# Kernel optimization log

Measured on AMD Instinct MI355X. Metric: run time of the kernel, lower is better.

Reference implementation:

```python
import jax, jax.numpy as jnp
import numpy as np

N, E, F_IN, HID, EMB = 100000, 3200000, 128, 16, 8
NEG_SLOPE = 0.2


def _seg_softmax(logits, seg, n):
    # Numerically stable softmax over segments (per trailing channel if 2D).
    m = jax.ops.segment_max(logits, seg, num_segments=n)
    e = jnp.exp(logits - m[seg])
    s = jax.ops.segment_sum(e, seg, num_segments=n)
    return e / s[seg]


def _gatv2(x, src, dst, Wl, Wr, att, bias, t, n):
    # GATv2Conv, heads=1, add_self_loops=False, eval mode (dropout off),
    # with learnable SoftmaxAggregation replacing the sum aggregation.
    xl = x @ Wl                      # [N, C] source transform
    xr = x @ Wr                      # [N, C] target transform
    score = jnp.sum(jax.nn.leaky_relu(xl[src] + xr[dst], NEG_SLOPE) * att, axis=-1)  # [E]
    alpha = _seg_softmax(score, dst, n)          # attention softmax over incoming edges
    m = xl[src] * alpha[:, None]                 # [E, C] messages
    w = _seg_softmax(m * t, dst, n)              # SoftmaxAggregation(learn=True), per channel
    return jax.ops.segment_sum(w * m, dst, num_segments=n) + bias


def setup_inputs() -> dict:
    key = jax.random.key(0)
    ks = iter(jax.random.split(key, 32))
    r = lambda shape, s=0.1: jax.random.normal(next(ks), shape, dtype=jnp.float32) * s
    return dict(
        x=r((N, F_IN), 1.0),
        edge_index=jax.random.randint(next(ks), (2, E), 0, N, dtype=jnp.int32),
        batch=jnp.arange(N, dtype=jnp.int32),
        Wl1=r((F_IN, HID)), Wr1=r((F_IN, HID)), att1=r((HID,)), b1=r((HID,)),
        Wlin1=r((F_IN, HID)), blin1=r((HID,)),
        Wl2=r((HID, EMB)), Wr2=r((HID, EMB)), att2=r((EMB,)), b2=r((EMB,)),
        Wlin2=r((HID, EMB)), blin2=r((EMB,)),
        t=jnp.ones((1,), jnp.float32),
        W3=r((EMB, EMB)), b3=r((EMB,)),
        W4=r((EMB, 1)), b4=r((1,)),
        W5=r((1, 1)), b5=r((1,)),
        Wout=r((1, 1)), bout=r((1,)),
    )


def reference(x, edge_index, batch, Wl1, Wr1, att1, b1, Wlin1, blin1,
              Wl2, Wr2, att2, b2, Wlin2, blin2, t,
              W3, b3, W4, b4, W5, b5, Wout, bout):
    n = x.shape[0]
    src, dst = edge_index[0], edge_index[1]
    # layer 1: GATv2 + skip Linear, relu, global_add_pool
    h = _gatv2(x, src, dst, Wl1, Wr1, att1, b1, t, n) + (x @ Wlin1 + blin1)
    h = jax.nn.relu(h)
    g = jax.ops.segment_sum(h, batch, num_segments=n)  # global_add_pool (batch=arange(N))
    # layer 2: GATv2 + skip Linear on pooled tensor (as in original code), relu, pool
    h2 = _gatv2(g, src, dst, Wl2, Wr2, att2, b2, t, n) + (g @ Wlin2 + blin2)
    h2 = jax.nn.relu(h2)
    g2 = jax.ops.segment_sum(h2, batch, num_segments=n)
    # small MLP head
    z = jax.nn.relu(g2 @ W3 + b3)
    z = jax.nn.relu(z @ W4 + b4)
    z = jax.nn.relu(z @ W5 + b5)
    return jax.nn.log_sigmoid(z @ Wout + bout)
```

## Files before the change

### kernel.cpp

```cpp
#include <hip/hip_runtime.h>
#include <hip/hip_bf16.h>
#include <math.h>

#define F_IN 128
#define C1 16
#define C2 8

#define LBITS 8
#define LOCAL (1 << LBITS)
#define NB_MAX 512
#define ITEMS 16
#define EPB (256 * ITEMS)

static __device__ __forceinline__ unsigned short f2bf(float f) {
  __hip_bfloat16 h = __float2bfloat16(f);
  return *(unsigned short*)&h;
}

__global__ void bucket_hist(const int* __restrict__ dst, int* __restrict__ bcount, int E, int NB) {
  __shared__ int h[NB_MAX];
  for (int i = threadIdx.x; i < NB; i += blockDim.x) h[i] = 0;
  __syncthreads();
  int stride = gridDim.x * blockDim.x;
  for (int e = blockIdx.x * blockDim.x + threadIdx.x; e < E; e += stride)
    atomicAdd(&h[dst[e] >> LBITS], 1);
  __syncthreads();
  for (int i = threadIdx.x; i < NB; i += blockDim.x)
    if (h[i]) atomicAdd(&bcount[i], h[i]);
}

__global__ void bucket_scan(const int* __restrict__ bcount, int* __restrict__ bbase,
                            int* __restrict__ bcursor, int NB) {
  __shared__ int sd[NB_MAX];
  int t = threadIdx.x;
  int v = (t < NB) ? bcount[t] : 0;
  sd[t] = v;
  __syncthreads();
  int acc = v;
  for (int off = 1; off < NB_MAX; off <<= 1) {
    int u = (t >= off) ? sd[t - off] : 0;
    __syncthreads();
    acc += u;
    sd[t] = acc;
    __syncthreads();
  }
  if (t < NB) {
    int excl = acc - v;
    bbase[t] = excl;
    bcursor[t] = excl;
    if (t == NB - 1) bbase[NB] = acc;
  }
}

__global__ __launch_bounds__(256) void phaseA_lds(const int* __restrict__ src,
                                                  const int* __restrict__ dst,
                                                  int* __restrict__ bcursor,
                                                  int* __restrict__ packed, int E, int NB) {
  __shared__ int hist[NB_MAX];
  __shared__ int lbase[NB_MAX];
  __shared__ int gbase[NB_MAX];
  __shared__ int sdata[256];
  __shared__ int stage[EPB];
  __shared__ unsigned short stageb[EPB];
  int t = threadIdx.x;
  for (int i = t; i < NB; i += 256) hist[i] = 0;
  __syncthreads();
  int base = blockIdx.x * EPB;
  int vals[ITEMS];
  int bkt[ITEMS];
#pragma unroll
  for (int k = 0; k < ITEMS; k++) {
    int e = base + k * 256 + t;
    if (e < E) {
      int s = src[e];
      int d = dst[e];
      bkt[k] = d >> LBITS;
      vals[k] = (s << LBITS) | (d & (LOCAL - 1));
      atomicAdd(&hist[bkt[k]], 1);
    } else {
      bkt[k] = -1;
    }
  }
  __syncthreads();
  int i0 = 2 * t, i1 = 2 * t + 1;
  int h0 = (i0 < NB) ? hist[i0] : 0;
  int h1 = (i1 < NB) ? hist[i1] : 0;
  int s2 = h0 + h1;
  sdata[t] = s2;
  __syncthreads();
  int acc = s2;
  for (int off = 1; off < 256; off <<= 1) {
    int u = (t >= off) ? sdata[t - off] : 0;
    __syncthreads();
    acc += u;
    sdata[t] = acc;
    __syncthreads();
  }
  int excl = acc - s2;
  if (i0 < NB) lbase[i0] = excl;
  if (i1 < NB) lbase[i1] = excl + h0;
  __syncthreads();
  for (int i = t; i < NB; i += 256) {
    int c = hist[i];
    gbase[i] = c ? atomicAdd(&bcursor[i], c) : 0;
    hist[i] = lbase[i];
  }
  __syncthreads();
#pragma unroll
  for (int k = 0; k < ITEMS; k++) {
    if (bkt[k] >= 0) {
      int lp = atomicAdd(&hist[bkt[k]], 1);
      stage[lp] = vals[k];
      stageb[lp] = (unsigned short)bkt[k];
    }
  }
  __syncthreads();
  int blockE = E - base;
  if (blockE > EPB) blockE = EPB;
  for (int i = t; i < blockE; i += 256) {
    int b = stageb[i];
    packed[gbase[b] + (i - lbase[b])] = stage[i];
  }
}

__global__ void phaseB_sort(const int* __restrict__ packed, const int* __restrict__ bbase,
                            int* __restrict__ row_ptr, int* __restrict__ ssrc, int N, int E) {
  __shared__ int h[LOCAL];
  __shared__ int sd[LOCAL];
  int b = blockIdx.x;
  int t = threadIdx.x;
  int beg = bbase[b], end = bbase[b + 1];
  int node0 = b << LBITS;
  h[t] = 0;
  __syncthreads();
  for (int j = beg + t; j < end; j += blockDim.x) atomicAdd(&h[packed[j] & (LOCAL - 1)], 1);
  __syncthreads();
  int cnt = h[t];
  sd[t] = cnt;
  __syncthreads();
  int acc = cnt;
  for (int off = 1; off < LOCAL; off <<= 1) {
    int u = (t >= off) ? sd[t - off] : 0;
    __syncthreads();
    acc += u;
    sd[t] = acc;
    __syncthreads();
  }
  int myex = acc - cnt;
  int node = node0 + t;
  if (node < N) row_ptr[node] = beg + myex;
  h[t] = beg + myex;
  if (b == gridDim.x - 1 && t == 0) row_ptr[N] = E;
  __syncthreads();
  for (int j = beg + t; j < end; j += blockDim.x) {
    int v = packed[j];
    int p = atomicAdd(&h[v & (LOCAL - 1)], 1);
    ssrc[p] = v >> LBITS;
  }
}

__global__ __launch_bounds__(256) void gemm3_128x16(
    const float* __restrict__ x, const float* __restrict__ Wl, const float* __restrict__ Wr,
    const float* __restrict__ Wlin, const float* __restrict__ blin,
    __hip_bfloat16* __restrict__ XLh, float* __restrict__ XR, float* __restrict__ SK, int N) {
  int bx = blockIdx.x;
  int mat = bx % 3;
  int node = (bx / 3) * 256 + threadIdx.x;
  if (node >= N) return;
  const float* __restrict__ W = (mat == 0) ? Wl : (mat == 1) ? Wr : Wlin;
  const float4* xr4 = (const float4*)(x + (size_t)node * F_IN);
  float acc[16];
#pragma unroll
  for (int c = 0; c < 16; c++) acc[c] = 0.f;
#pragma unroll 8
  for (int kk = 0; kk < F_IN / 4; kk++) {
    float4 xv = xr4[kk];
    float xs[4] = {xv.x, xv.y, xv.z, xv.w};
#pragma unroll
    for (int j = 0; j < 4; j++) {
      int k = kk * 4 + j;
#pragma unroll
      for (int c = 0; c < 16; c++) acc[c] = fmaf(xs[j], W[k * 16 + c], acc[c]);
    }
  }
  if (mat == 0) {
    unsigned int pk[8];
#pragma unroll
    for (int i = 0; i < 8; i++)
      pk[i] = (unsigned)f2bf(acc[2 * i]) | ((unsigned)f2bf(acc[2 * i + 1]) << 16);
    uint4* xlp = (uint4*)(XLh + (size_t)node * 16);
    xlp[0] = make_uint4(pk[0], pk[1], pk[2], pk[3]);
    xlp[1] = make_uint4(pk[4], pk[5], pk[6], pk[7]);
  } else if (mat == 1) {
    float4* xrp = (float4*)(XR + (size_t)node * 16);
#pragma unroll
    for (int q = 0; q < 4; q++)
      xrp[q] = make_float4(acc[4 * q], acc[4 * q + 1], acc[4 * q + 2], acc[4 * q + 3]);
  } else {
    float4* skp = (float4*)(SK + (size_t)node * 16);
#pragma unroll
    for (int q = 0; q < 4; q++)
      skp[q] = make_float4(acc[4 * q] + blin[4 * q], acc[4 * q + 1] + blin[4 * q + 1],
                           acc[4 * q + 2] + blin[4 * q + 2], acc[4 * q + 3] + blin[4 * q + 3]);
  }
}

template <int C, int POOL, bool HEAD, bool FUSEG2>
__global__ __launch_bounds__(256) void gat_layer(
    const __hip_bfloat16* __restrict__ XLh, const float* __restrict__ XR,
    const float* __restrict__ SK, const float* __restrict__ att, const float* __restrict__ bias,
    const float* __restrict__ tp, const int* __restrict__ row_ptr, const int* __restrict__ ssrc,
    float* __restrict__ H, int N,
    const float* __restrict__ P0, const float* __restrict__ P1, const float* __restrict__ P2,
    const float* __restrict__ P3, const float* __restrict__ P4, const float* __restrict__ P5,
    const float* __restrict__ P6, const float* __restrict__ P7,
    __hip_bfloat16* __restrict__ XL2h, float* __restrict__ XR2, float* __restrict__ SK2,
    float* __restrict__ out) {
  constexpr int NPB = 256 / C;
  constexpr int LOGNPB = (NPB == 16) ? 4 : 5;
  __shared__ __align__(16) unsigned short vpool[POOL * C];
  __shared__ float ppool[POOL];
  __shared__ __align__(16) float xrl[NPB * C];
  __shared__ float invS0s[NPB];
  __shared__ int nb[NPB + 1];
  __shared__ float hsh[(HEAD || FUSEG2) ? NPB * C : 1];
  __shared__ float wfuse[FUSEG2 ? 392 : 1];
  int t = threadIdx.x;
  int node0 = blockIdx.x * NPB;

  if (t <= NPB) {
    int nd = node0 + t;
    nb[t] = row_ptr[(nd < N) ? nd : N];
  }
  {
    size_t xi = (size_t)node0 * C + t;
    xrl[t] = (xi < (size_t)N * C) ? XR[xi] : 0.f;
  }
  if constexpr (FUSEG2) {
    for (int i = t; i < 392; i += 256)
      wfuse[i] = (i < 128) ? P0[i] : (i < 256) ? P1[i - 128] : (i < 384) ? P2[i - 256] : P3[i - 384];
  }
  float attr[C];
#pragma unroll
  for (int cc = 0; cc < C; cc++) attr[cc] = att[cc];
  float tval = tp[0];
  __syncthreads();

  int bbeg = nb[0];
  int nE = nb[NPB] - bbeg;
  int nCap = (nE < POOL) ? nE : POOL;
  const unsigned short* XLu = (const unsigned short*)XLh;

  for (int slot = t; slot < nCap; slot += 256) {
    int sb = slot + bbeg;
    int lo = 0, hi = NPB;
#pragma unroll
    for (int st = 0; st < LOGNPB; st++) {
      int mid = (lo + hi) >> 1;
      bool go = nb[mid] <= sb;
      lo = go ? mid : lo;
      hi = go ? hi : mid;
    }
    int g = lo;
    int s = ssrc[sb];
    float v[C];
    if constexpr (C == 16) {
      const uint4* gp = (const uint4*)(XLu + (size_t)s * 16);
      uint4 a = gp[0], b = gp[1];
      *(uint4*)&vpool[slot * 16] = a;
      *(uint4*)&vpool[slot * 16 + 8] = b;
      unsigned arr[8] = {a.x, a.y, a.z, a.w, b.x, b.y, b.z, b.w};
#pragma unroll
      for (int i = 0; i < 8; i++) {
        v[2 * i] = __uint_as_float(arr[i] << 16);
        v[2 * i + 1] = __uint_as_float(arr[i] & 0xffff0000u);
      }
    } else {
      const uint4* gp = (const uint4*)(XLu + (size_t)s * 8);
      uint4 a = gp[0];
      *(uint4*)&vpool[slot * 8] = a;
      unsigned arr[4] = {a.x, a.y, a.z, a.w};
#pragma unroll
      for (int i = 0; i < 4; i++) {
        v[2 * i] = __uint_as_float(arr[i] << 16);
        v[2 * i + 1] = __uint_as_float(arr[i] & 0xffff0000u);
      }
    }
    float xr[C];
    const float4* xp = (const float4*)&xrl[g * C];
#pragma unroll
    for (int q = 0; q < C / 4; q++) {
      float4 f = xp[q];
      xr[4 * q] = f.x;
      xr[4 * q + 1] = f.y;
      xr[4 * q + 2] = f.z;
      xr[4 * q + 3] = f.w;
    }
    float p0 = 0.f, p1 = 0.f, p2 = 0.f, p3 = 0.f;
#pragma unroll
    for (int cc = 0; cc < C; cc += 4) {
      float u0 = v[cc] + xr[cc];
      float u1 = v[cc + 1] + xr[cc + 1];
      float u2 = v[cc + 2] + xr[cc + 2];
      float u3 = v[cc + 3] + xr[cc + 3];
      p0 = fmaf(fmaxf(u0, 0.2f * u0), attr[cc], p0);
      p1 = fmaf(fmaxf(u1, 0.2f * u1), attr[cc + 1], p1);
      p2 = fmaf(fmaxf(u2, 0.2f * u2), attr[cc + 2], p2);
      p3 = fmaf(fmaxf(u3, 0.2f * u3), attr[cc + 3], p3);
    }
    ppool[slot] = __expf((p0 + p1) + (p2 + p3));
  }
  __syncthreads();

  int g = t / C;
  int c = t % C;
  int base = nb[g] - bbeg;
  int deg = nb[g + 1] - nb[g];
  int capd = POOL - base;
  capd = capd < 0 ? 0 : (capd > deg ? deg : capd);

  {
    float s0 = 0.f;
    for (int j = c; j < capd; j += C) s0 += ppool[base + j];
    for (int j = capd + c; j < deg; j += C) {
      int s = ssrc[bbeg + base + j];
      float sc = 0.f;
#pragma unroll
      for (int cc = 0; cc < C; cc++) {
        float v = __bfloat162float(XLh[(size_t)s * C + cc]);
        float u = v + xrl[g * C + cc];
        sc = fmaf(fmaxf(u, 0.2f * u), attr[cc], sc);
      }
      s0 += __expf(sc);
    }
#pragma unroll
    for (int m = 1; m < C; m <<= 1) s0 += __shfl_xor(s0, m, C);
    if (c == 0) invS0s[g] = (deg > 0) ? 1.0f / s0 : 0.f;
  }
  __syncthreads();

  float invS0 = invS0s[g];
  float S1 = 0.f, S2 = 0.f, S1b = 0.f, S2b = 0.f;
  int jj = 0;
  for (; jj + 2 <= capd; jj += 2) {
    int sl0 = base + jj;
    float v0 = __uint_as_float(((unsigned)vpool[sl0 * C + c]) << 16);
    float p0 = ppool[sl0];
    float v1 = __uint_as_float(((unsigned)vpool[(sl0 + 1) * C + c]) << 16);
    float p1 = ppool[sl0 + 1];
    float m0 = v0 * (p0 * invS0);
    float m1 = v1 * (p1 * invS0);
    float w0 = __expf(m0 * tval);
    float w1 = __expf(m1 * tval);
    S1 += w0;
    S2 = fmaf(w0, m0, S2);
    S1b += w1;
    S2b = fmaf(w1, m1, S2b);
  }
  for (; jj < capd; jj++) {
    int sl = base + jj;
    float v = __uint_as_float(((unsigned)vpool[sl * C + c]) << 16);
    float p = ppool[sl];
    float mm = v * (p * invS0);
    float w = __expf(mm * tval);
    S1 += w;
    S2 = fmaf(w, mm, S2);
  }
  for (; jj < deg; jj++) {
    int s = ssrc[bbeg + base + jj];
    float sc = 0.f, vc = 0.f;
#pragma unroll
    for (int cc = 0; cc < C; cc++) {
      float v = __bfloat162float(XLh[(size_t)s * C + cc]);
      if (cc == c) vc = v;
      float u = v + xrl[g * C + cc];
      sc = fmaf(fmaxf(u, 0.2f * u), attr[cc], sc);
    }
    float p = __expf(sc);
    float mm = vc * (p * invS0);
    float w = __expf(mm * tval);
    S1 += w;
    S2 = fmaf(w, mm, S2);
  }
  S1 += S1b;
  S2 += S2b;

  int node = node0 + g;
  bool valid = node < N;
  float hval = 0.f;
  if (valid) {
    float gat = (deg > 0) ? (S2 / S1) : 0.f;
    hval = fmaxf(gat + bias[c] + SK[(size_t)node * C + c], 0.f);
  }
  if constexpr (FUSEG2) {
    hsh[g * C + c] = hval;
    __syncthreads();
    if (t < NPB * 8) {
      int g2 = t >> 3, c2 = t & 7;
      int nd = node0 + g2;
      if (nd < N) {
        float a0 = 0.f, a1 = 0.f, a2 = 0.f;
#pragma unroll
        for (int k = 0; k < 16; k++) {
          float hv = hsh[g2 * 16 + k];
          a0 = fmaf(hv, wfuse[k * 8 + c2], a0);
          a1 = fmaf(hv, wfuse[128 + k * 8 + c2], a1);
          a2 = fmaf(hv, wfuse[256 + k * 8 + c2], a2);
        }
        ((unsigned short*)XL2h)[(size_t)nd * 8 + c2] = f2bf(a0);
        XR2[(size_t)nd * 8 + c2] = a1;
        SK2[(size_t)nd * 8 + c2] = a2 + wfuse[384 + c2];
      }
    }
  } else if constexpr (HEAD) {
    hsh[g * C + c] = hval;
    __syncthreads();
    if (t < NPB) {
      int nd = node0 + t;
      if (nd < N) {
        float h[8];
#pragma unroll
        for (int k = 0; k < 8; k++) h[k] = hsh[t * 8 + k];
        float s4 = 0.f;
#pragma unroll
        for (int cc = 0; cc < 8; cc++) {
          float z = P1[cc];
#pragma unroll
          for (int k = 0; k < 8; k++) z = fmaf(h[k], P0[k * 8 + cc], z);
          z = fmaxf(z, 0.f);
          s4 = fmaf(z, P2[cc], s4);
        }
        s4 = fmaxf(s4 + P3[0], 0.f);
        float s5 = fmaxf(fmaf(s4, P4[0], P5[0]), 0.f);
        float zo = fmaf(s5, P6[0], P7[0]);
        float ls;
        if (zo >= 0.f)
          ls = -log1pf(expf(-zo));
        else
          ls = zo - log1pf(expf(zo));
        out[nd] = ls;
      }
    }
  } else {
    if (valid) H[(size_t)node * C + c] = hval;
  }
}

extern "C" void kernel_launch(void* const* d_in, const int* in_sizes, int n_in,
                              void* d_out, int out_size, void* d_ws, size_t ws_size,
                              hipStream_t stream) {
  const float* x = (const float*)d_in[0];
  const int* ei = (const int*)d_in[1];
  const float* Wl1 = (const float*)d_in[3];
  const float* Wr1 = (const float*)d_in[4];
  const float* att1 = (const float*)d_in[5];
  const float* b1 = (const float*)d_in[6];
  const float* Wlin1 = (const float*)d_in[7];
  const float* blin1 = (const float*)d_in[8];
  const float* Wl2 = (const float*)d_in[9];
  const float* Wr2 = (const float*)d_in[10];
  const float* att2 = (const float*)d_in[11];
  const float* b2 = (const float*)d_in[12];
  const float* Wlin2 = (const float*)d_in[13];
  const float* blin2 = (const float*)d_in[14];
  const float* t = (const float*)d_in[15];
  const float* W3 = (const float*)d_in[16];
  const float* b3 = (const float*)d_in[17];
  const float* W4 = (const float*)d_in[18];
  const float* b4 = (const float*)d_in[19];
  const float* W5 = (const float*)d_in[20];
  const float* b5 = (const float*)d_in[21];
  const float* Wout = (const float*)d_in[22];
  const float* bout = (const float*)d_in[23];
  float* out = (float*)d_out;

  int N = in_sizes[0] / F_IN;
  int E = in_sizes[1] / 2;
  const int* src = ei;
  const int* dst = ei + E;
  int NB = (N + LOCAL - 1) >> LBITS;

  char* ws = (char*)d_ws;
  size_t off = 0;
  auto alloc = [&](size_t bytes) -> void* {
    void* p = ws + off;
    off = (off + bytes + 255) & ~(size_t)255;
    return p;
  };
  int* bcount = (int*)alloc((size_t)NB * 4);
  int* bbase = (int*)alloc((size_t)(NB + 1) * 4);
  int* bcursor = (int*)alloc((size_t)NB * 4);
  int* packed = (int*)alloc((size_t)E * 4);
  int* row_ptr = (int*)alloc((size_t)(N + 1) * 4);
  int* ssrc = (int*)alloc((size_t)E * 4);
  __hip_bfloat16* XL1 = (__hip_bfloat16*)alloc((size_t)N * C1 * 2);
  float* XR1 = (float*)alloc((size_t)N * C1 * 4);
  float* SK1 = (float*)alloc((size_t)N * C1 * 4);
  __hip_bfloat16* XL2 = (__hip_bfloat16*)alloc((size_t)N * C2 * 2);
  float* XR2 = (float*)alloc((size_t)N * C2 * 4);
  float* SK2 = (float*)alloc((size_t)N * C2 * 4);

  int nblkA = (E + EPB - 1) / EPB;
  int nodeBlk = (N + 255) / 256;

  hipMemsetAsync(bcount, 0, (size_t)NB * 4, stream);
  hipLaunchKernelGGL(bucket_hist, dim3(512), dim3(256), 0, stream, dst, bcount, E, NB);
  hipLaunchKernelGGL(bucket_scan, dim3(1), dim3(NB_MAX), 0, stream, bcount, bbase, bcursor, NB);
  hipLaunchKernelGGL(phaseA_lds, dim3(nblkA), dim3(256), 0, stream, src, dst, bcursor, packed, E,
                     NB);
  hipLaunchKernelGGL(phaseB_sort, dim3(NB), dim3(LOCAL), 0, stream, packed, bbase, row_ptr, ssrc, N,
                     E);
  hipLaunchKernelGGL(gemm3_128x16, dim3(nodeBlk * 3), dim3(256), 0, stream, x, Wl1, Wr1,
                     Wlin1, blin1, XL1, XR1, SK1, N);
  hipLaunchKernelGGL((gat_layer<16, 640, false, true>), dim3((N + 15) / 16), dim3(256), 0, stream,
                     XL1, XR1, SK1, att1, b1, t, row_ptr, ssrc, nullptr, N, Wl2, Wr2, Wlin2, blin2,
                     nullptr, nullptr, nullptr, nullptr, XL2, XR2, SK2, nullptr);
  hipLaunchKernelGGL((gat_layer<8, 1280, true, false>), dim3((N + 31) / 32), dim3(256), 0, stream,
                     XL2, XR2, SK2, att2, b2, t, row_ptr, ssrc, nullptr, N, W3, b3, W4, b4, W5, b5,
                     Wout, bout, nullptr, nullptr, nullptr, out);
}
```

Measured before the change: 309.9 us.

## Pack local node id into sorted sources and fold softmax scaling into pool

Result: no change. 311.2 us (+0.4%).

```diff
diff --git a/kernel.cpp b/kernel.cpp
--- a/kernel.cpp
+++ b/kernel.cpp
@@ -22,8 +22,20 @@
   for (int i = threadIdx.x; i < NB; i += blockDim.x) h[i] = 0;
   __syncthreads();
   int stride = gridDim.x * blockDim.x;
-  for (int e = blockIdx.x * blockDim.x + threadIdx.x; e < E; e += stride)
-    atomicAdd(&h[dst[e] >> LBITS], 1);
+  int tid = blockIdx.x * blockDim.x + threadIdx.x;
+  if ((E & 3) == 0) {
+    const int4* d4 = (const int4*)dst;
+    int n4 = E >> 2;
+    for (int i = tid; i < n4; i += stride) {
+      int4 d = d4[i];
+      atomicAdd(&h[d.x >> LBITS], 1);
+      atomicAdd(&h[d.y >> LBITS], 1);
+      atomicAdd(&h[d.z >> LBITS], 1);
+      atomicAdd(&h[d.w >> LBITS], 1);
+    }
+  } else {
+    for (int e = tid; e < E; e += stride) atomicAdd(&h[dst[e] >> LBITS], 1);
+  }
   __syncthreads();
   for (int i = threadIdx.x; i < NB; i += blockDim.x)
     if (h[i]) atomicAdd(&bcount[i], h[i]);
@@ -68,17 +80,38 @@
   int base = blockIdx.x * EPB;
   int vals[ITEMS];
   int bkt[ITEMS];
-#pragma unroll
-  for (int k = 0; k < ITEMS; k++) {
-    int e = base + k * 256 + t;
-    if (e < E) {
-      int s = src[e];
-      int d = dst[e];
-      bkt[k] = d >> LBITS;
-      vals[k] = (s << LBITS) | (d & (LOCAL - 1));
-      atomicAdd(&hist[bkt[k]], 1);
-    } else {
-      bkt[k] = -1;
+  bool vec = ((E & 3) == 0) && (base + EPB <= E);
+  if (vec) {
+    const int4* s4 = (const int4*)(src + base);
+    const int4* d4 = (const int4*)(dst + base);
+#pragma unroll
+    for (int q = 0; q < ITEMS / 4; q++) {
+      int idx = q * 256 + t;
+      int4 sv = s4[idx];
+      int4 dv = d4[idx];
+      int ss[4] = {sv.x, sv.y, sv.z, sv.w};
+      int dd[4] = {dv.x, dv.y, dv.z, dv.w};
+#pragma unroll
+      for (int r = 0; r < 4; r++) {
+        int k = q * 4 + r;
+        bkt[k] = dd[r] >> LBITS;
+        vals[k] = (ss[r] << LBITS) | (dd[r] & (LOCAL - 1));
+        atomicAdd(&hist[bkt[k]], 1);
+      }
+    }
+  } else {
+#pragma unroll
+    for (int k = 0; k < ITEMS; k++) {
+      int e = base + k * 256 + t;
+      if (e < E) {
+        int s = src[e];
+        int d = dst[e];
+        bkt[k] = d >> LBITS;
+        vals[k] = (s << LBITS) | (d & (LOCAL - 1));
+        atomicAdd(&hist[bkt[k]], 1);
+      } else {
+        bkt[k] = -1;
+      }
     }
   }
   __syncthreads();
@@ -106,12 +139,21 @@
     hist[i] = lbase[i];
   }
   __syncthreads();
-#pragma unroll
-  for (int k = 0; k < ITEMS; k++) {
-    if (bkt[k] >= 0) {
+  if (vec) {
+#pragma unroll
+    for (int k = 0; k < ITEMS; k++) {
       int lp = atomicAdd(&hist[bkt[k]], 1);
       stage[lp] = vals[k];
       stageb[lp] = (unsigned short)bkt[k];
+    }
+  } else {
+#pragma unroll
+    for (int k = 0; k < ITEMS; k++) {
+      if (bkt[k] >= 0) {
+        int lp = atomicAdd(&hist[bkt[k]], 1);
+        stage[lp] = vals[k];
+        stageb[lp] = (unsigned short)bkt[k];
+      }
     }
   }
   __syncthreads();
@@ -154,8 +196,9 @@
   __syncthreads();
   for (int j = beg + t; j < end; j += blockDim.x) {
     int v = packed[j];
-    int p = atomicAdd(&h[v & (LOCAL - 1)], 1);
-    ssrc[p] = v >> LBITS;
+    int l = v & (LOCAL - 1);
+    int p = atomicAdd(&h[l], 1);
+    ssrc[p] = ((v >> LBITS) << 5) | (l & 31);
   }
 }
 
@@ -217,11 +260,9 @@
     __hip_bfloat16* __restrict__ XL2h, float* __restrict__ XR2, float* __restrict__ SK2,
     float* __restrict__ out) {
   constexpr int NPB = 256 / C;
-  constexpr int LOGNPB = (NPB == 16) ? 4 : 5;
   __shared__ __align__(16) unsigned short vpool[POOL * C];
   __shared__ float ppool[POOL];
   __shared__ __align__(16) float xrl[NPB * C];
-  __shared__ float invS0s[NPB];
   __shared__ int nb[NPB + 1];
   __shared__ float hsh[(HEAD || FUSEG2) ? NPB * C : 1];
   __shared__ float wfuse[FUSEG2 ? 392 : 1];
@@ -252,17 +293,9 @@
   const unsigned short* XLu = (const unsigned short*)XLh;
 
   for (int slot = t; slot < nCap; slot += 256) {
-    int sb = slot + bbeg;
-    int lo = 0, hi = NPB;
-#pragma unroll
-    for (int st = 0; st < LOGNPB; st++) {
-      int mid = (lo + hi) >> 1;
-      bool go = nb[mid] <= sb;
-      lo = go ? mid : lo;
-      hi = go ? hi : mid;
-    }
-    int g = lo;
-    int s = ssrc[sb];
+    int sp = ssrc[bbeg + slot];
+    int s = sp >> 5;
+    int g = sp & (NPB - 1);
     float v[C];
     if constexpr (C == 16) {
       const uint4* gp = (const uint4*)(XLu + (size_t)s * 16);
@@ -319,11 +352,12 @@
   int capd = POOL - base;
   capd = capd < 0 ? 0 : (capd > deg ? deg : capd);
 
+  float invS0;
   {
     float s0 = 0.f;
     for (int j = c; j < capd; j += C) s0 += ppool[base + j];
     for (int j = capd + c; j < deg; j += C) {
-      int s = ssrc[bbeg + base + j];
+      int s = ssrc[bbeg + base + j] >> 5;
       float sc = 0.f;
 #pragma unroll
       for (int cc = 0; cc < C; cc++) {
@@ -335,39 +369,36 @@
     }
 #pragma unroll
     for (int m = 1; m < C; m <<= 1) s0 += __shfl_xor(s0, m, C);
-    if (c == 0) invS0s[g] = (deg > 0) ? 1.0f / s0 : 0.f;
-  }
-  __syncthreads();
-
-  float invS0 = invS0s[g];
+    invS0 = (deg > 0) ? 1.0f / s0 : 0.f;
+    float a = invS0 * tval;
+    for (int j = c; j < capd; j += C) ppool[base + j] *= a;
+  }
+
   float S1 = 0.f, S2 = 0.f, S1b = 0.f, S2b = 0.f;
   int jj = 0;
   for (; jj + 2 <= capd; jj += 2) {
     int sl0 = base + jj;
     float v0 = __uint_as_float(((unsigned)vpool[sl0 * C + c]) << 16);
-    float p0 = ppool[sl0];
+    float q0 = v0 * ppool[sl0];
     float v1 = __uint_as_float(((unsigned)vpool[(sl0 + 1) * C + c]) << 16);
-    float p1 = ppool[sl0 + 1];
-    float m0 = v0 * (p0 * invS0);
-    float m1 = v1 * (p1 * invS0);
-    float w0 = __expf(m0 * tval);
-    float w1 = __expf(m1 * tval);
+    float q1 = v1 * ppool[sl0 + 1];
+    float w0 = __expf(q0);
+    float w1 = __expf(q1);
     S1 += w0;
-    S2 = fmaf(w0, m0, S2);
+    S2 = fmaf(w0, q0, S2);
     S1b += w1;
-    S2b = fmaf(w1, m1, S2b);
+    S2b = fmaf(w1, q1, S2b);
   }
   for (; jj < capd; jj++) {
     int sl = base + jj;
     float v = __uint_as_float(((unsigned)vpool[sl * C + c]) << 16);
-    float p = ppool[sl];
-    float mm = v * (p * invS0);
-    float w = __expf(mm * tval);
+    float q = v * ppool[sl];
+    float w = __expf(q);
     S1 += w;
-    S2 = fmaf(w, mm, S2);
+    S2 = fmaf(w, q, S2);
   }
   for (; jj < deg; jj++) {
-    int s = ssrc[bbeg + base + jj];
+    int s = ssrc[bbeg + base + jj] >> 5;
     float sc = 0.f, vc = 0.f;
 #pragma unroll
     for (int cc = 0; cc < C; cc++) {
@@ -377,10 +408,10 @@
       sc = fmaf(fmaxf(u, 0.2f * u), attr[cc], sc);
     }
     float p = __expf(sc);
-    float mm = vc * (p * invS0);
-    float w = __expf(mm * tval);
+    float q = vc * (p * invS0 * tval);
+    float w = __expf(q);
     S1 += w;
-    S2 = fmaf(w, mm, S2);
+    S2 = fmaf(w, q, S2);
   }
   S1 += S1b;
   S2 += S2b;
@@ -389,7 +420,8 @@
   bool valid = node < N;
   float hval = 0.f;
   if (valid) {
-    float gat = (deg > 0) ? (S2 / S1) : 0.f;
+    float td = (tval != 0.f) ? tval : 1.f;
+    float gat = (deg > 0) ? (S2 / (S1 * td)) : 0.f;
     hval = fmaxf(gat + bias[c] + SK[(size_t)node * C + c], 0.f);
   }
   if constexpr (FUSEG2) {
@@ -504,7 +536,7 @@
   int nodeBlk = (N + 255) / 256;
 
   hipMemsetAsync(bcount, 0, (size_t)NB * 4, stream);
-  hipLaunchKernelGGL(bucket_hist, dim3(512), dim3(256), 0, stream, dst, bcount, E, NB);
+  hipLaunchKernelGGL(bucket_hist, dim3(1024), dim3(256), 0, stream, dst, bcount, E, NB);
   hipLaunchKernelGGL(bucket_scan, dim3(1), dim3(NB_MAX), 0, stream, bcount, bbase, bcursor, NB);
   hipLaunchKernelGGL(phaseA_lds, dim3(nblkA), dim3(256), 0, stream, src, dst, bcursor, packed, E,
                      NB);
@@ -515,7 +547,7 @@
   hipLaunchKernelGGL((gat_layer<16, 640, false, true>), dim3((N + 15) / 16), dim3(256), 0, stream,
                      XL1, XR1, SK1, att1, b1, t, row_ptr, ssrc, nullptr, N, Wl2, Wr2, Wlin2, blin2,
                      nullptr, nullptr, nullptr, nullptr, XL2, XR2, SK2, nullptr);
-  hipLaunchKernelGGL((gat_layer<8, 1280, true, false>), dim3((N + 31) / 32), dim3(256), 0, stream,
+  hipLaunchKernelGGL((gat_layer<8, 1216, true, false>), dim3((N + 31) / 32), dim3(256), 0, stream,
                      XL2, XR2, SK2, att2, b2, t, row_ptr, ssrc, nullptr, N, W3, b3, W4, b4, W5, b5,
                      Wout, bout, nullptr, nullptr, nullptr, out);
 }
```
